# Kernel tuning notes

Measured on AMD Instinct MI355X. Metric: run time of the kernel, lower is better.

The kernel has to match this reference:

```python
import jax, jax.numpy as jnp
import numpy as np

N, B, T, E = 16384, 8, 32, 262144
D, H = 256, 8
HD = D // H

def _ln(x, g, b, eps=1e-5):
    m = x.mean(-1, keepdims=True)
    va = x.var(-1, keepdims=True)
    return (x - m) * jax.lax.rsqrt(va + eps) * g + b

def setup_inputs():
    key = jax.random.key(0)
    ks = jax.random.split(key, 40)
    rn = lambda i, sh, s=0.02: jax.random.normal(ks[i], sh, jnp.float32) * s
    inp = {}
    inp['x'] = jax.random.normal(ks[0], (N, D), jnp.float32)
    inp['edge_index'] = jax.random.randint(ks[1], (2, E), 0, N)
    inp['edge_attr'] = jax.random.normal(ks[2], (E, D), jnp.float32)
    inp['v'] = jax.random.normal(ks[3], (B, T, D), jnp.float32)
    inp['batch'] = jnp.sort(jax.random.randint(ks[4], (N,), 0, B))
    ones = lambda sh: jnp.ones(sh, jnp.float32)
    zeros = lambda sh: jnp.zeros(sh, jnp.float32)
    # LayerNorms
    inp['n1_g'], inp['n1_b'] = ones((D,)), zeros((D,))
    inp['vn_g'], inp['vn_b'] = ones((D,)), zeros((D,))
    inp['n3_g'], inp['n3_b'] = ones((D,)), zeros((D,))
    inp['n4_g'], inp['n4_b'] = ones((D,)), zeros((D,))
    # GINEConv: eps (train_eps, init 0) + MLP [D, 2D, D] with layer_norm+gelu on hidden
    inp['gine_eps'] = jnp.float32(0.0)
    inp['g_w1'], inp['g_b1'] = rn(5, (2 * D, D)), zeros((2 * D,))
    inp['g_lng'], inp['g_lnb'] = ones((2 * D,)), zeros((2 * D,))
    inp['g_w2'], inp['g_b2'] = rn(6, (D, 2 * D)), zeros((D,))
    # GatedResidual gammas (init 1e-5)
    inp['gamma1'] = jnp.full((D,), 1e-5, jnp.float32)
    inp['gamma2'] = jnp.full((D,), 1e-5, jnp.float32)
    inp['gamma3'] = jnp.full((D,), 1e-5, jnp.float32)
    # MultiheadAttention (packed in_proj)
    inp['mha_in_w'], inp['mha_in_b'] = rn(7, (3 * D, D)), zeros((3 * D,))
    inp['mha_out_w'], inp['mha_out_b'] = rn(8, (D, D)), zeros((D,))
    # node->token cross attention projections
    inp['q_w'], inp['q_b'] = rn(9, (D, D)), zeros((D,))
    inp['kv_w'], inp['kv_b'] = rn(10, (2 * D, D)), zeros((2 * D,))
    inp['o_w'], inp['o_b'] = rn(11, (D, D)), zeros((D,))
    # FFN MLP [D, 4D, D] (eval-mode batch_norm == identity with default stats)
    inp['f_w1'], inp['f_b1'] = rn(12, (4 * D, D)), zeros((4 * D,))
    inp['f_w2'], inp['f_b2'] = rn(13, (D, 4 * D)), zeros((D,))
    return inp

def reference(x, edge_index, edge_attr, v, batch,
              n1_g, n1_b, vn_g, vn_b, n3_g, n3_b, n4_g, n4_b,
              gine_eps, g_w1, g_b1, g_lng, g_lnb, g_w2, g_b2,
              gamma1, gamma2, gamma3,
              mha_in_w, mha_in_b, mha_out_w, mha_out_b,
              q_w, q_b, kv_w, kv_b, o_w, o_b,
              f_w1, f_b1, f_w2, f_b2):
    scale = HD ** -0.5
    gelu = lambda t: jax.nn.gelu(t, approximate=False)
    # --- GINEConv on norm1(x) ---
    xn = _ln(x, n1_g, n1_b)
    src, dst = edge_index[0], edge_index[1]
    msg = jax.nn.relu(xn[src] + edge_attr)                      # [E, D]
    agg = jax.ops.segment_sum(msg, dst, num_segments=N)         # [N, D]
    hin = (1.0 + gine_eps) * xn + agg
    h = gelu(_ln(hin @ g_w1.T + g_b1, g_lng, g_lnb)) @ g_w2.T + g_b2
    x = x + gamma1 * h                                          # res1 (drop_path off in eval)
    # --- token self-attention with node summary context ---
    v_res = v
    vn = _ln(v, vn_g, vn_b)
    cnt = jnp.maximum(jax.ops.segment_sum(jnp.ones((N,), x.dtype), batch, num_segments=B), 1.0)
    node_summary = jax.ops.segment_sum(x, batch, num_segments=B) / cnt[:, None]  # [B, D]
    ctx = jnp.concatenate([vn, node_summary[:, None, :]], axis=1)                # [B, T+1, D]
    wq, wk, wv = jnp.split(mha_in_w, 3, axis=0)
    bq, bk, bv = jnp.split(mha_in_b, 3, axis=0)
    qh = (vn @ wq.T + bq).reshape(B, T, H, HD)
    kh = (ctx @ wk.T + bk).reshape(B, T + 1, H, HD)
    vh = (ctx @ wv.T + bv).reshape(B, T + 1, H, HD)
    a = jax.nn.softmax(jnp.einsum('bqhd,bkhd->bhqk', qh, kh) * scale, axis=-1)
    v_upd = jnp.einsum('bhqk,bkhd->bqhd', a, vh).reshape(B, T, D) @ mha_out_w.T + mha_out_b
    v = v_res + gamma2 * v_upd                                  # res2
    # --- node -> token cross attention (gather-expand KV by batch) ---
    xn3 = _ln(x, n3_g, n3_b)
    q = (xn3 @ q_w.T + q_b).reshape(N, H, HD)
    kv = (v @ kv_w.T + kv_b).reshape(B, T, 2, H, HD)
    k, val = kv[:, :, 0], kv[:, :, 1]                           # [B, T, H, HD]
    k_exp, val_exp = k[batch], val[batch]                       # [N, T, H, HD]
    scores = jnp.einsum('nhd,nthd->nht', q, k_exp) * scale
    attn = jax.nn.softmax(scores, axis=-1)                      # scatter_softmax w/ all-zero idx == softmax over t
    attn_out = jnp.einsum('nht,nthd->nhd', attn, val_exp).reshape(N, D)
    x = x + gamma3 * (attn_out @ o_w.T + o_b)                   # res3
    # --- FFN ---
    xn4 = _ln(x, n4_g, n4_b)
    x = x + (gelu(xn4 @ f_w1.T + f_b1) @ f_w2.T + f_b2)
    return (x, v)
```

## Files before the change

### kernel.cpp

```cpp
#include <hip/hip_runtime.h>
#include <math.h>

#define NN 16384
#define EE 262144
#define BB 8
#define TT 32
#define DD 256
#define HH 8
#define HDD 32

typedef __bf16 bf16;
typedef __bf16 bf16x8 __attribute__((ext_vector_type(8)));
typedef __bf16 bf16x4 __attribute__((ext_vector_type(4)));
typedef float f32x4 __attribute__((ext_vector_type(4)));

#define GM_F32 0
#define GM_BF16 1
#define GM_GELU 2
#define GM_RES 3
#define GM_RES2 4

__device__ __forceinline__ float gelu_f(float v) {
  return 0.5f * v * (1.f + erff(v * 0.70710678118654752440f));
}

__device__ __forceinline__ void ln256(const float* __restrict__ xr,
                                      const float* __restrict__ g,
                                      const float* __restrict__ bb,
                                      bf16* __restrict__ o, float* red) {
  int t = threadIdx.x;
  float v = xr[t];
  float s = v, s2 = v * v;
#pragma unroll
  for (int off = 32; off > 0; off >>= 1) {
    s += __shfl_down(s, off, 64);
    s2 += __shfl_down(s2, off, 64);
  }
  int wv = t >> 6;
  if ((t & 63) == 0) { red[wv] = s; red[4 + wv] = s2; }
  __syncthreads();
  s = red[0] + red[1] + red[2] + red[3];
  s2 = red[4] + red[5] + red[6] + red[7];
  float m = s * (1.f / 256.f);
  float rs = rsqrtf(s2 * (1.f / 256.f) - m * m + 1e-5f);
  o[t] = (bf16)((v - m) * rs * g[t] + bb[t]);
}

struct Pro {
  const float* wsrc[9];
  bf16* wdst[9];
  int wblk[10];
  const float* x; const float* n1_g; const float* n1_b; bf16* xn;
  const float* v; const float* vn_g; const float* vn_b; bf16* vn;
  const int* batch; float* cntf;
  const int* ei; int* deg;
};

__global__ __launch_bounds__(256) void prologue(Pro p) {
  __shared__ float red[8];
  __shared__ int hist[BB];
  int b = blockIdx.x, t = threadIdx.x;
  if (b < 1280) {
    int s = 0;
    while (b >= p.wblk[s + 1]) ++s;
    int i = (b - p.wblk[s]) * 1024 + t * 4;
    const float4 f = *(const float4*)(p.wsrc[s] + i);
    bf16x4 o;
    o[0] = (bf16)f.x; o[1] = (bf16)f.y; o[2] = (bf16)f.z; o[3] = (bf16)f.w;
    *(bf16x4*)(p.wdst[s] + i) = o;
  } else if (b < 17664) {
    size_t r = b - 1280;
    ln256(p.x + r * 256, p.n1_g, p.n1_b, p.xn + r * 256, red);
  } else if (b < 17920) {
    size_t r = b - 17664;
    ln256(p.v + r * 256, p.vn_g, p.vn_b, p.vn + r * 256, red);
  } else if (b < 17984) {
    if (t < BB) hist[t] = 0;
    __syncthreads();
    int n = (b - 17920) * 256 + t;
    atomicAdd(&hist[p.batch[n]], 1);
    __syncthreads();
    if (t < BB) {
      int h = hist[t];
      if (h) atomicAdd(&p.cntf[t], (float)h);
    }
  } else {
    int e = (b - 17984) * 256 + t;
    atomicAdd(&p.deg[p.ei[EE + e]], 1);
  }
}

__global__ __launch_bounds__(1024) void scan16k(const int* __restrict__ deg,
                                                int* __restrict__ offs, int* __restrict__ woff) {
  __shared__ int part[1024];
  int t = threadIdx.x;
  int base = t * 16;
  int v[16];
  int s = 0;
#pragma unroll
  for (int j = 0; j < 16; ++j) { v[j] = deg[base + j]; s += v[j]; }
  part[t] = s;
  __syncthreads();
  for (int o = 1; o < 1024; o <<= 1) {
    int x = (t >= o) ? part[t - o] : 0;
    __syncthreads();
    part[t] += x;
    __syncthreads();
  }
  int excl = part[t] - s;
#pragma unroll
  for (int j = 0; j < 16; ++j) {
    offs[base + j] = excl;
    woff[base + j] = excl;
    excl += v[j];
  }
  if (t == 1023) offs[NN] = part[1023];
}

struct GemmP {
  const bf16* A; const bf16* W; const float* bias;
  int M, K, NC, mode;
  const float* res; const float* gamma;
  float* outf; bf16* outb;
};

__device__ __forceinline__ void gemm_core(const GemmP p, int bx, int by) {
  int wave = threadIdx.x >> 6;
  int lane = threadIdx.x & 63;
  int qd = lane >> 4;
  int l16 = lane & 15;
  int r0 = by * 128 + wave * 32;
  int c0 = bx * 64;
  int ar0 = r0 + l16;       if (ar0 >= p.M) ar0 = p.M - 1;
  int ar1 = r0 + 16 + l16;  if (ar1 >= p.M) ar1 = p.M - 1;
  const bf16* Ap0 = p.A + (size_t)ar0 * p.K + qd * 8;
  const bf16* Ap1 = p.A + (size_t)ar1 * p.K + qd * 8;
  const bf16* Wp = p.W + (size_t)(c0 + l16) * p.K + qd * 8;
  size_t K16 = (size_t)16 * p.K;
  f32x4 acc00 = {0.f, 0.f, 0.f, 0.f};
  f32x4 acc01 = acc00, acc02 = acc00, acc03 = acc00;
  f32x4 acc10 = acc00, acc11 = acc00, acc12 = acc00, acc13 = acc00;
  bf16x8 a0, a1, b0, b1, b2, b3, na0, na1, nb0, nb1, nb2, nb3;

#define GLOADS(A0, A1, B0, B1, B2, B3, kk)                \
  A0 = *(const bf16x8*)(Ap0 + (kk));                      \
  A1 = *(const bf16x8*)(Ap1 + (kk));                      \
  B0 = *(const bf16x8*)(Wp + (kk));                       \
  B1 = *(const bf16x8*)(Wp + K16 + (kk));                 \
  B2 = *(const bf16x8*)(Wp + 2 * K16 + (kk));             \
  B3 = *(const bf16x8*)(Wp + 3 * K16 + (kk));
#define GMFMAS(A0, A1, B0, B1, B2, B3)                                  \
  acc00 = __builtin_amdgcn_mfma_f32_16x16x32_bf16(A0, B0, acc00, 0, 0, 0); \
  acc01 = __builtin_amdgcn_mfma_f32_16x16x32_bf16(A0, B1, acc01, 0, 0, 0); \
  acc02 = __builtin_amdgcn_mfma_f32_16x16x32_bf16(A0, B2, acc02, 0, 0, 0); \
  acc03 = __builtin_amdgcn_mfma_f32_16x16x32_bf16(A0, B3, acc03, 0, 0, 0); \
  acc10 = __builtin_amdgcn_mfma_f32_16x16x32_bf16(A1, B0, acc10, 0, 0, 0); \
  acc11 = __builtin_amdgcn_mfma_f32_16x16x32_bf16(A1, B1, acc11, 0, 0, 0); \
  acc12 = __builtin_amdgcn_mfma_f32_16x16x32_bf16(A1, B2, acc12, 0, 0, 0); \
  acc13 = __builtin_amdgcn_mfma_f32_16x16x32_bf16(A1, B3, acc13, 0, 0, 0);

  GLOADS(a0, a1, b0, b1, b2, b3, 0)
  int k = 32;
  for (; k + 32 < p.K; k += 64) {
    GLOADS(na0, na1, nb0, nb1, nb2, nb3, k)
    GMFMAS(a0, a1, b0, b1, b2, b3)
    GLOADS(a0, a1, b0, b1, b2, b3, k + 32)
    GMFMAS(na0, na1, nb0, nb1, nb2, nb3)
  }
  GLOADS(na0, na1, nb0, nb1, nb2, nb3, k)
  GMFMAS(a0, a1, b0, b1, b2, b3)
  GMFMAS(na0, na1, nb0, nb1, nb2, nb3)
#undef GLOADS
#undef GMFMAS

  f32x4 accs[2][4] = {{acc00, acc01, acc02, acc03}, {acc10, acc11, acc12, acc13}};
#pragma unroll
  for (int s = 0; s < 2; ++s) {
#pragma unroll
    for (int c = 0; c < 4; ++c) {
      int col = c0 + c * 16 + l16;
      float bv = p.bias[col];
#pragma unroll
      for (int i = 0; i < 4; ++i) {
        int row = r0 + s * 16 + qd * 4 + i;
        if (row >= p.M) continue;
        size_t idx = (size_t)row * p.NC + col;
        float v = accs[s][c][i] + bv;
        if (p.mode == GM_F32) p.outf[idx] = v;
        else if (p.mode == GM_BF16) p.outb[idx] = (bf16)v;
        else if (p.mode == GM_GELU) p.outb[idx] = (bf16)gelu_f(v);
        else {
          float g = p.gamma ? p.gamma[col] : 1.f;
          float r = p.res[idx] + g * v;
          p.outf[idx] = r;
          if (p.mode == GM_RES2) p.outb[idx] = (bf16)r;
        }
      }
    }
  }
}

__global__ __launch_bounds__(256) void gemm_one(GemmP p, int nbx) {
  gemm_core(p, blockIdx.x % nbx, blockIdx.x / nbx);
}

__global__ __launch_bounds__(256) void csr_fill_qh(const int* __restrict__ ei,
                                                   int* __restrict__ woff,
                                                   int2* __restrict__ csr2, GemmP qp) {
  int b = blockIdx.x;
  if (b < 1024) {
    int e = b * 256 + threadIdx.x;
    int d = ei[EE + e];
    int s = ei[e];
    int p = atomicAdd(&woff[d], 1);
    csr2[p] = make_int2(e, s);
  } else {
    int l = b - 1024;
    gemm_core(qp, l % 4, l / 4);
  }
}

__global__ __launch_bounds__(256) void gine_agg(const float* __restrict__ eattr,
                                                const bf16* __restrict__ xn,
                                                const int* __restrict__ offs,
                                                const int2* __restrict__ csr2,
                                                const float* __restrict__ epsp,
                                                bf16* __restrict__ hin) {
  __shared__ f32x4 red[4][64];
  int n = blockIdx.x;
  int wave = threadIdx.x >> 6, lane = threadIdx.x & 63;
  int s0 = offs[n], s1 = offs[n + 1];
  f32x4 acc = {0.f, 0.f, 0.f, 0.f};
  int i = s0 + wave;
  int2 es = (i < s1) ? csr2[i] : make_int2(0, 0);
  for (; i < s1; i += 4) {
    int2 cur = es;
    int inext = i + 4;
    if (inext < s1) es = csr2[inext];
    float4 ea = *(const float4*)(eattr + (size_t)cur.x * DD + lane * 4);
    bf16x4 xv = *(const bf16x4*)(xn + (size_t)cur.y * DD + lane * 4);
    acc[0] += fmaxf((float)xv[0] + ea.x, 0.f);
    acc[1] += fmaxf((float)xv[1] + ea.y, 0.f);
    acc[2] += fmaxf((float)xv[2] + ea.z, 0.f);
    acc[3] += fmaxf((float)xv[3] + ea.w, 0.f);
  }
  red[wave][lane] = acc;
  __syncthreads();
  if (wave == 0) {
    f32x4 a = red[0][lane];
    f32x4 a1 = red[1][lane], a2 = red[2][lane], a3 = red[3][lane];
    bf16x4 xs = *(const bf16x4*)(xn + (size_t)n * DD + lane * 4);
    float e1 = 1.f + epsp[0];
    bf16x4 o;
#pragma unroll
    for (int j = 0; j < 4; ++j)
      o[j] = (bf16)(e1 * (float)xs[j] + a[j] + a1[j] + a2[j] + a3[j]);
    *(bf16x4*)(hin + (size_t)n * DD + lane * 4) = o;
  }
}

__global__ __launch_bounds__(256) void gemm_g1_ln(const bf16* __restrict__ A,
                                                  const bf16* __restrict__ W,
                                                  const float* __restrict__ bias,
                                                  const float* __restrict__ lng,
                                                  const float* __restrict__ lnb,
                                                  bf16* __restrict__ out) {
  __shared__ float ssum[4][32], ssum2[4][32], smm[32], smr[32];
  int w = threadIdx.x >> 6, lane = threadIdx.x & 63;
  int qd = lane >> 4, l16 = lane & 15;
  int r0 = blockIdx.x * 32;
  int c0 = w * 128;
  const bf16* Ap0 = A + (size_t)(r0 + l16) * 256 + qd * 8;
  const bf16* Ap1 = Ap0 + (size_t)16 * 256;
  const bf16* Wp = W + (size_t)(c0 + l16) * 256 + qd * 8;
  f32x4 z = {0.f, 0.f, 0.f, 0.f};
  f32x4 acc0[8], acc1[8];
#pragma unroll
  for (int cf = 0; cf < 8; ++cf) { acc0[cf] = z; acc1[cf] = z; }
  for (int k = 0; k < 256; k += 32) {
    bf16x8 a0 = *(const bf16x8*)(Ap0 + k);
    bf16x8 a1 = *(const bf16x8*)(Ap1 + k);
#pragma unroll
    for (int cf = 0; cf < 8; ++cf) {
      bf16x8 bv = *(const bf16x8*)(Wp + (size_t)cf * 16 * 256 + k);
      acc0[cf] = __builtin_amdgcn_mfma_f32_16x16x32_bf16(a0, bv, acc0[cf], 0, 0, 0);
      acc1[cf] = __builtin_amdgcn_mfma_f32_16x16x32_bf16(a1, bv, acc1[cf], 0, 0, 0);
    }
  }
#pragma unroll
  for (int cf = 0; cf < 8; ++cf) {
    float bv = bias[c0 + cf * 16 + l16];
#pragma unroll
    for (int i = 0; i < 4; ++i) { acc0[cf][i] += bv; acc1[cf][i] += bv; }
  }
#pragma unroll
  for (int s = 0; s < 2; ++s) {
#pragma unroll
    for (int i = 0; i < 4; ++i) {
      float ps = 0.f, ps2 = 0.f;
#pragma unroll
      for (int cf = 0; cf < 8; ++cf) {
        float v = s ? acc1[cf][i] : acc0[cf][i];
        ps += v; ps2 += v * v;
      }
#pragma unroll
      for (int off = 8; off > 0; off >>= 1) {
        ps += __shfl_down(ps, off, 16);
        ps2 += __shfl_down(ps2, off, 16);
      }
      if (l16 == 0) { int rib = s * 16 + qd * 4 + i; ssum[w][rib] = ps; ssum2[w][rib] = ps2; }
    }
  }
  __syncthreads();
  if (threadIdx.x < 32) {
    int rib = threadIdx.x;
    float S = ssum[0][rib] + ssum[1][rib] + ssum[2][rib] + ssum[3][rib];
    float S2 = ssum2[0][rib] + ssum2[1][rib] + ssum2[2][rib] + ssum2[3][rib];
    float m = S * (1.f / 512.f);
    smm[rib] = m;
    smr[rib] = rsqrtf(S2 * (1.f / 512.f) - m * m + 1e-5f);
  }
  __syncthreads();
#pragma unroll
  for (int s = 0; s < 2; ++s) {
#pragma unroll
    for (int cf = 0; cf < 8; ++cf) {
      int col = c0 + cf * 16 + l16;
      float g = lng[col], b = lnb[col];
#pragma unroll
      for (int i = 0; i < 4; ++i) {
        int rib = s * 16 + qd * 4 + i;
        float v = ((s ? acc1[cf][i] : acc0[cf][i]) - smm[rib]) * smr[rib] * g + b;
        out[(size_t)(r0 + rib) * 512 + col] = (bf16)gelu_f(v);
      }
    }
  }
}

struct ResLnP {
  const bf16* A; const bf16* W; const float* bias;
  const float* res; const float* gamma;
  float* resout; const float* lng; const float* lnb; bf16* lnout;
  int K; int seg; const int* batch; float* summary;
};

__global__ __launch_bounds__(256) void gemm_res_ln(ResLnP p) {
  __shared__ float ssum[4][32], ssum2[4][32], smm[32], smr[32];
  int w = threadIdx.x >> 6, lane = threadIdx.x & 63;
  int qd = lane >> 4, l16 = lane & 15;
  int r0 = blockIdx.x * 32;
  int c0 = w * 64;
  const bf16* Ap0 = p.A + (size_t)(r0 + l16) * p.K + qd * 8;
  const bf16* Ap1 = Ap0 + (size_t)16 * p.K;
  const bf16* Wp = p.W + (size_t)(c0 + l16) * p.K + qd * 8;
  size_t K16 = (size_t)16 * p.K;
  f32x4 z = {0.f, 0.f, 0.f, 0.f};
  f32x4 acc0[4], acc1[4];
#pragma unroll
  for (int cf = 0; cf < 4; ++cf) { acc0[cf] = z; acc1[cf] = z; }
  for (int k = 0; k < p.K; k += 32) {
    bf16x8 a0 = *(const bf16x8*)(Ap0 + k);
    bf16x8 a1 = *(const bf16x8*)(Ap1 + k);
#pragma unroll
    for (int cf = 0; cf < 4; ++cf) {
      bf16x8 bv = *(const bf16x8*)(Wp + cf * K16 + k);
      acc0[cf] = __builtin_amdgcn_mfma_f32_16x16x32_bf16(a0, bv, acc0[cf], 0, 0, 0);
      acc1[cf] = __builtin_amdgcn_mfma_f32_16x16x32_bf16(a1, bv, acc1[cf], 0, 0, 0);
    }
  }
  float rr0[4][4], rr1[4][4];
#pragma unroll
  for (int cf = 0; cf < 4; ++cf) {
    int col = c0 + cf * 16 + l16;
    float bv = p.bias[col], gm = p.gamma[col];
#pragma unroll
    for (int i = 0; i < 4; ++i) {
      {
        int row = r0 + qd * 4 + i;
        size_t idx = (size_t)row * 256 + col;
        float r = p.res[idx] + gm * (acc0[cf][i] + bv);
        p.resout[idx] = r; rr0[cf][i] = r;
      }
      {
        int row = r0 + 16 + qd * 4 + i;
        size_t idx = (size_t)row * 256 + col;
        float r = p.res[idx] + gm * (acc1[cf][i] + bv);
        p.resout[idx] = r; rr1[cf][i] = r;
      }
    }
  }
#pragma unroll
  for (int s = 0; s < 2; ++s) {
#pragma unroll
    for (int i = 0; i < 4; ++i) {
      float ps = 0.f, ps2 = 0.f;
#pragma unroll
      for (int cf = 0; cf < 4; ++cf) {
        float v = s ? rr1[cf][i] : rr0[cf][i];
        ps += v; ps2 += v * v;
      }
#pragma unroll
      for (int off = 8; off > 0; off >>= 1) {
        ps += __shfl_down(ps, off, 16);
        ps2 += __shfl_down(ps2, off, 16);
      }
      if (l16 == 0) { int rib = s * 16 + qd * 4 + i; ssum[w][rib] = ps; ssum2[w][rib] = ps2; }
    }
  }
  __syncthreads();
  if (threadIdx.x < 32) {
    int rib = threadIdx.x;
    float S = ssum[0][rib] + ssum[1][rib] + ssum[2][rib] + ssum[3][rib];
    float S2 = ssum2[0][rib] + ssum2[1][rib] + ssum2[2][rib] + ssum2[3][rib];
    float m = S * (1.f / 256.f);
    smm[rib] = m;
    smr[rib] = rsqrtf(S2 * (1.f / 256.f) - m * m + 1e-5f);
  }
  __syncthreads();
#pragma unroll
  for (int cf = 0; cf < 4; ++cf) {
    int col = c0 + cf * 16 + l16;
    float lg = p.lng[col], lb = p.lnb[col];
#pragma unroll
    for (int i = 0; i < 4; ++i) {
      {
        int rib = qd * 4 + i;
        p.lnout[(size_t)(r0 + rib) * 256 + col] =
            (bf16)((rr0[cf][i] - smm[rib]) * smr[rib] * lg + lb);
      }
      {
        int rib = 16 + qd * 4 + i;
        p.lnout[(size_t)(r0 + rib) * 256 + col] =
            (bf16)((rr1[cf][i] - smm[rib]) * smr[rib] * lg + lb);
      }
    }
  }
  if (p.seg) {
    int b0 = p.batch[r0], b31 = p.batch[r0 + 31];
    if (b0 == b31) {
#pragma unroll
      for (int cf = 0; cf < 4; ++cf) {
        float sl = 0.f;
#pragma unroll
        for (int i = 0; i < 4; ++i) sl += rr0[cf][i] + rr1[cf][i];
        sl += __shfl_xor(sl, 16, 64);
        sl += __shfl_xor(sl, 32, 64);
        if (qd == 0) atomicAdd(&p.summary[(size_t)b0 * 256 + c0 + cf * 16 + l16], sl);
      }
    } else {
#pragma unroll
      for (int cf = 0; cf < 4; ++cf) {
        int col = c0 + cf * 16 + l16;
#pragma unroll
        for (int i = 0; i < 4; ++i) {
          atomicAdd(&p.summary[(size_t)p.batch[r0 + qd * 4 + i] * 256 + col], rr0[cf][i]);
          atomicAdd(&p.summary[(size_t)p.batch[r0 + 16 + qd * 4 + i] * 256 + col], rr1[cf][i]);
        }
      }
    }
  }
}

__global__ __launch_bounds__(256) void mid2(const float* __restrict__ summary,
                                            const float* __restrict__ cntf,
                                            const bf16* __restrict__ vn,
                                            bf16* __restrict__ ctx,
                                            GemmP qp) {
  int b = blockIdx.x, t = threadIdx.x;
  if (b < BB * (TT + 1)) {
    int bb = b / (TT + 1), k = b % (TT + 1);
    float val;
    if (k < TT) val = (float)vn[((size_t)(bb * TT + k)) * DD + t];
    else val = summary[(size_t)bb * DD + t] / fmaxf(cntf[bb], 1.f);
    ctx[(size_t)b * DD + t] = (bf16)val;
  } else {
    int l = b - BB * (TT + 1);
    gemm_core(qp, l % 4, l / 4);
  }
}

__global__ __launch_bounds__(256) void mha_small(const float* __restrict__ qh,
                                                 const float* __restrict__ kvh,
                                                 bf16* __restrict__ vatt) {
  int b = blockIdx.x;
  int h = threadIdx.x >> 5, qi = threadIdx.x & 31;
  const float scale = 0.17677669529663687f;
  float sc[TT + 1];
  float mx = -1e30f;
  const float* qp = qh + ((size_t)(b * TT + qi)) * DD + h * HDD;
#pragma unroll
  for (int k = 0; k < TT + 1; ++k) {
    const float* kp = kvh + ((size_t)(b * (TT + 1) + k)) * 512 + h * HDD;
    float s = 0.f;
#pragma unroll
    for (int d = 0; d < HDD; ++d) s += qp[d] * kp[d];
    s *= scale;
    sc[k] = s;
    mx = fmaxf(mx, s);
  }
  float sum = 0.f;
#pragma unroll
  for (int k = 0; k < TT + 1; ++k) {
    sc[k] = __expf(sc[k] - mx);
    sum += sc[k];
  }
  float inv = 1.f / sum;
#pragma unroll
  for (int d = 0; d < HDD; ++d) {
    float o = 0.f;
#pragma unroll
    for (int k = 0; k < TT + 1; ++k)
      o += sc[k] * kvh[((size_t)(b * (TT + 1) + k)) * 512 + 256 + h * HDD + d];
    vatt[((size_t)(b * TT + qi)) * DD + h * HDD + d] = (bf16)(o * inv);
  }
}

__global__ __launch_bounds__(256) void cross_attn(const bf16* __restrict__ qx,
                                                  const float* __restrict__ kvx,
                                                  const int* __restrict__ batch,
                                                  bf16* __restrict__ attnout) {
  __shared__ float v_lds[TT * DD];
  int tid = threadIdx.x;
  int n0 = blockIdx.x * 16;
  int b0 = batch[n0];
  for (int i = tid; i < TT * DD; i += 256) {
    int t = i >> 8, c = i & 255;
    v_lds[i] = kvx[((size_t)(b0 * TT + t)) * 512 + 256 + c];
  }
  int h = tid >> 5, lt = tid & 31;
  float kreg[HDD];
  {
    const float* kp = kvx + ((size_t)(b0 * TT + lt)) * 512 + h * HDD;
#pragma unroll
    for (int d = 0; d < HDD; ++d) kreg[d] = kp[d];
  }
  __syncthreads();
  const float scale = 0.17677669529663687f;
  for (int ni = 0; ni < 16; ++ni) {
    int n = n0 + ni;
    int b = batch[n];
    const bf16* qp = qx + (size_t)n * DD + h * HDD;
    float s = 0.f;
    if (b == b0) {
#pragma unroll
      for (int d = 0; d < HDD; ++d) s += (float)qp[d] * kreg[d];
    } else {
      const float* kp = kvx + ((size_t)(b * TT + lt)) * 512 + h * HDD;
#pragma unroll
      for (int d = 0; d < HDD; ++d) s += (float)qp[d] * kp[d];
    }
    s *= scale;
    float mx = s;
#pragma unroll
    for (int o = 16; o > 0; o >>= 1) mx = fmaxf(mx, __shfl_xor(mx, o, 32));
    float e = __expf(s - mx);
    float sum = e;
#pragma unroll
    for (int o = 16; o > 0; o >>= 1) sum += __shfl_xor(sum, o, 32);
    float a = e / sum;
    float o_acc = 0.f;
    int base_lane = (h & 1) << 5;
    if (b == b0) {
#pragma unroll
      for (int t = 0; t < TT; ++t) {
        float at = __shfl(a, base_lane + t, 64);
        o_acc += at * v_lds[t * DD + h * HDD + lt];
      }
    } else {
#pragma unroll
      for (int t = 0; t < TT; ++t) {
        float at = __shfl(a, base_lane + t, 64);
        o_acc += at * kvx[((size_t)(b * TT + t)) * 512 + 256 + h * HDD + lt];
      }
    }
    attnout[(size_t)n * DD + h * HDD + lt] = (bf16)o_acc;
  }
}

extern "C" void kernel_launch(void* const* d_in, const int* in_sizes, int n_in,
                              void* d_out, int out_size, void* d_ws, size_t ws_size,
                              hipStream_t stream) {
  const float* x = (const float*)d_in[0];
  const int* ei = (const int*)d_in[1];
  const float* eattr = (const float*)d_in[2];
  const float* v = (const float*)d_in[3];
  const int* batch = (const int*)d_in[4];
  const float* n1_g = (const float*)d_in[5];
  const float* n1_b = (const float*)d_in[6];
  const float* vn_g = (const float*)d_in[7];
  const float* vn_b = (const float*)d_in[8];
  const float* n3_g = (const float*)d_in[9];
  const float* n3_b = (const float*)d_in[10];
  const float* n4_g = (const float*)d_in[11];
  const float* n4_b = (const float*)d_in[12];
  const float* gine_eps = (const float*)d_in[13];
  const float* g_w1 = (const float*)d_in[14];
  const float* g_b1 = (const float*)d_in[15];
  const float* g_lng = (const float*)d_in[16];
  const float* g_lnb = (const float*)d_in[17];
  const float* g_w2 = (const float*)d_in[18];
  const float* g_b2 = (const float*)d_in[19];
  const float* gamma1 = (const float*)d_in[20];
  const float* gamma2 = (const float*)d_in[21];
  const float* gamma3 = (const float*)d_in[22];
  const float* mha_in_w = (const float*)d_in[23];
  const float* mha_in_b = (const float*)d_in[24];
  const float* mha_out_w = (const float*)d_in[25];
  const float* mha_out_b = (const float*)d_in[26];
  const float* q_w = (const float*)d_in[27];
  const float* q_b = (const float*)d_in[28];
  const float* kv_w = (const float*)d_in[29];
  const float* kv_b = (const float*)d_in[30];
  const float* o_w = (const float*)d_in[31];
  const float* o_b = (const float*)d_in[32];
  const float* f_w1 = (const float*)d_in[33];
  const float* f_b1 = (const float*)d_in[34];
  const float* f_w2 = (const float*)d_in[35];
  const float* f_b2 = (const float*)d_in[36];

  float* out_x = (float*)d_out;
  float* out_v = (float*)d_out + (size_t)NN * DD;

  char* wsp = (char*)d_ws;
  size_t off = 0;
  auto alloc = [&](size_t bytes) -> void* {
    void* p = wsp + off;
    off += (bytes + 255) & ~(size_t)255;
    return p;
  };
  float* t1f = (float*)alloc(33554432);
  bf16* u_bf = (bf16*)t1f;
  bf16* xn_bf = (bf16*)alloc(8388608);
  bf16* qx_bf = xn_bf;
  bf16* t1g_bf = (bf16*)alloc(16777216);
  float* x2f = (float*)t1g_bf;
  float* x1f = (float*)alloc(16777216);
  bf16* hin_bf = (bf16*)alloc(8388608);
  bf16* xn3_bf = hin_bf;
  bf16* att_bf = (bf16*)alloc(8388608);
  bf16* xn4_bf = att_bf;
  int* deg = (int*)alloc(NN * 4);
  float* summary = (float*)alloc(BB * DD * 4);
  float* cntf = (float*)alloc(BB * 4);
  int* offs = (int*)alloc((NN + 1) * 4);
  int* woff = (int*)alloc(NN * 4);
  int2* csr2 = (int2*)alloc((size_t)EE * 8);
  bf16* vn_bf = (bf16*)alloc(BB * TT * DD * 2);
  bf16* ctx_bf = (bf16*)alloc(BB * (TT + 1) * DD * 2);
  float* qhf = (float*)alloc(BB * TT * DD * 4);
  float* kvhf = (float*)alloc(BB * (TT + 1) * 512 * 4);
  bf16* vatt_bf = (bf16*)alloc(BB * TT * DD * 2);
  bf16* vout_bf = (bf16*)alloc(BB * TT * DD * 2);
  float* kvxf = (float*)alloc(BB * TT * 512 * 4);
  bf16* wbuf = (bf16*)alloc((size_t)1310720 * 2);

  bf16* g_w1b = wbuf;
  bf16* g_w2b = g_w1b + 131072;
  bf16* mha_in_wb = g_w2b + 131072;
  bf16* q_wb = mha_in_wb + 196608;
  bf16* kv_wb = q_wb + 65536;
  bf16* o_wb = kv_wb + 131072;
  bf16* f_w1b = o_wb + 65536;
  bf16* f_w2b = f_w1b + 262144;
  bf16* mha_out_wb = f_w2b + 262144;

  hipMemsetAsync(deg, 0, NN * 4 + BB * DD * 4 + 256, stream);

  Pro pr;
  pr.wsrc[0] = g_w1; pr.wdst[0] = g_w1b;
  pr.wsrc[1] = g_w2; pr.wdst[1] = g_w2b;
  pr.wsrc[2] = mha_in_w; pr.wdst[2] = mha_in_wb;
  pr.wsrc[3] = mha_out_w; pr.wdst[3] = mha_out_wb;
  pr.wsrc[4] = q_w; pr.wdst[4] = q_wb;
  pr.wsrc[5] = kv_w; pr.wdst[5] = kv_wb;
  pr.wsrc[6] = o_w; pr.wdst[6] = o_wb;
  pr.wsrc[7] = f_w1; pr.wdst[7] = f_w1b;
  pr.wsrc[8] = f_w2; pr.wdst[8] = f_w2b;
  int bs[10] = {0, 128, 256, 448, 512, 576, 704, 768, 1024, 1280};
  for (int i = 0; i < 10; ++i) pr.wblk[i] = bs[i];
  pr.x = x; pr.n1_g = n1_g; pr.n1_b = n1_b; pr.xn = xn_bf;
  pr.v = v; pr.vn_g = vn_g; pr.vn_b = vn_b; pr.vn = vn_bf;
  pr.batch = batch; pr.cntf = cntf;
  pr.ei = ei; pr.deg = deg;
  prologue<<<19008, 256, 0, stream>>>(pr);

  scan16k<<<1, 1024, 0, stream>>>(deg, offs, woff);

  GemmP j_qh = {vn_bf, mha_in_wb, mha_in_b, BB * TT, 256, 256, GM_F32,
                nullptr, nullptr, qhf, nullptr};
  csr_fill_qh<<<1024 + 8, 256, 0, stream>>>(ei, woff, csr2, j_qh);

  gine_agg<<<NN, 256, 0, stream>>>(eattr, xn_bf, offs, csr2, gine_eps, hin_bf);

  gemm_g1_ln<<<NN / 32, 256, 0, stream>>>(hin_bf, g_w1b, g_b1, g_lng, g_lnb, t1g_bf);

  ResLnP j_g2 = {t1g_bf, g_w2b, g_b2, x, gamma1, x1f, n3_g, n3_b, xn3_bf,
                 512, 1, batch, summary};
  gemm_res_ln<<<NN / 32, 256, 0, stream>>>(j_g2);

  GemmP j_q = {xn3_bf, q_wb, q_b, NN, 256, 256, GM_BF16, nullptr, nullptr, nullptr, qx_bf};
  mid2<<<BB * (TT + 1) + 512, 256, 0, stream>>>(summary, cntf, vn_bf, ctx_bf, j_q);

  GemmP j_kvh = {ctx_bf, mha_in_wb + (size_t)256 * 256, mha_in_b + 256, BB * (TT + 1), 256, 512,
                 GM_F32, nullptr, nullptr, kvhf, nullptr};
  gemm_one<<<24, 256, 0, stream>>>(j_kvh, 8);

  mha_small<<<BB, 256, 0, stream>>>(qhf, kvhf, vatt_bf);

  GemmP j_mo = {vatt_bf, mha_out_wb, mha_out_b, BB * TT, 256, 256, GM_RES2, v, gamma2, out_v, vout_bf};
  gemm_one<<<8, 256, 0, stream>>>(j_mo, 4);

  GemmP j_kv = {vout_bf, kv_wb, kv_b, BB * TT, 256, 512, GM_F32, nullptr, nullptr, kvxf, nullptr};
  gemm_one<<<16, 256, 0, stream>>>(j_kv, 8);

  cross_attn<<<NN / 16, 256, 0, stream>>>(qx_bf, kvxf, batch, att_bf);

  ResLnP j_o = {att_bf, o_wb, o_b, x1f, gamma3, x2f, n4_g, n4_b, xn4_bf,
                256, 0, nullptr, nullptr};
  gemm_res_ln<<<NN / 32, 256, 0, stream>>>(j_o);

  GemmP j_f1 = {xn4_bf, f_w1b, f_b1, NN, 256, 1024, GM_GELU, nullptr, nullptr, nullptr, u_bf};
  gemm_one<<<2048, 256, 0, stream>>>(j_f1, 16);

  GemmP j_f2 = {u_bf, f_w2b, f_b2, NN, 1024, 256, GM_RES, x2f, nullptr, out_x, nullptr};
  gemm_one<<<512, 256, 0, stream>>>(j_f2, 4);
}
```

Baseline: 914.1 us.

## Fuse FFN GEMMs via LDS, use wave-per-row LN and aggregation

Merges the two FFN GEMMs into one kernel that keeps the GELU hidden tile (32x1024 bf16) in shared memory, so the hidden activation never goes through global memory. The prologue LayerNorm now gives each wave one row with float4 loads and shuffle-only reductions, dropping the block-level sync. gine_agg gives each wave one node, removing the LDS cross-wave reduction. The trade-offs are about 66KB of LDS per block and 32 accumulator vectors per thread, which lowers occupancy. Per-node aggregation also becomes serial within a wave, so high-degree nodes have less parallelism.

```diff
diff --git a/kernel.cpp b/kernel.cpp
--- a/kernel.cpp
+++ b/kernel.cpp
@@ -24,26 +24,29 @@
   return 0.5f * v * (1.f + erff(v * 0.70710678118654752440f));
 }
 
-__device__ __forceinline__ void ln256(const float* __restrict__ xr,
-                                      const float* __restrict__ g,
-                                      const float* __restrict__ bb,
-                                      bf16* __restrict__ o, float* red) {
-  int t = threadIdx.x;
-  float v = xr[t];
-  float s = v, s2 = v * v;
+__device__ __forceinline__ void ln256w(const float* __restrict__ xr,
+                                       const float* __restrict__ g,
+                                       const float* __restrict__ bb,
+                                       bf16* __restrict__ o) {
+  int lane = threadIdx.x & 63;
+  float4 v = *(const float4*)(xr + lane * 4);
+  float s = v.x + v.y + v.z + v.w;
+  float s2 = v.x * v.x + v.y * v.y + v.z * v.z + v.w * v.w;
 #pragma unroll
   for (int off = 32; off > 0; off >>= 1) {
-    s += __shfl_down(s, off, 64);
-    s2 += __shfl_down(s2, off, 64);
-  }
-  int wv = t >> 6;
-  if ((t & 63) == 0) { red[wv] = s; red[4 + wv] = s2; }
-  __syncthreads();
-  s = red[0] + red[1] + red[2] + red[3];
-  s2 = red[4] + red[5] + red[6] + red[7];
+    s += __shfl_xor(s, off, 64);
+    s2 += __shfl_xor(s2, off, 64);
+  }
   float m = s * (1.f / 256.f);
   float rs = rsqrtf(s2 * (1.f / 256.f) - m * m + 1e-5f);
-  o[t] = (bf16)((v - m) * rs * g[t] + bb[t]);
+  float4 gg = *(const float4*)(g + lane * 4);
+  float4 bv = *(const float4*)(bb + lane * 4);
+  bf16x4 ov;
+  ov[0] = (bf16)((v.x - m) * rs * gg.x + bv.x);
+  ov[1] = (bf16)((v.y - m) * rs * gg.y + bv.y);
+  ov[2] = (bf16)((v.z - m) * rs * gg.z + bv.z);
+  ov[3] = (bf16)((v.w - m) * rs * gg.w + bv.w);
+  *(bf16x4*)(o + lane * 4) = ov;
 }
 
 struct Pro {
@@ -57,9 +60,9 @@
 };
 
 __global__ __launch_bounds__(256) void prologue(Pro p) {
-  __shared__ float red[8];
   __shared__ int hist[BB];
   int b = blockIdx.x, t = threadIdx.x;
+  int wave = t >> 6;
   if (b < 1280) {
     int s = 0;
     while (b >= p.wblk[s + 1]) ++s;
@@ -68,16 +71,16 @@
     bf16x4 o;
     o[0] = (bf16)f.x; o[1] = (bf16)f.y; o[2] = (bf16)f.z; o[3] = (bf16)f.w;
     *(bf16x4*)(p.wdst[s] + i) = o;
-  } else if (b < 17664) {
-    size_t r = b - 1280;
-    ln256(p.x + r * 256, p.n1_g, p.n1_b, p.xn + r * 256, red);
-  } else if (b < 17920) {
-    size_t r = b - 17664;
-    ln256(p.v + r * 256, p.vn_g, p.vn_b, p.vn + r * 256, red);
-  } else if (b < 17984) {
+  } else if (b < 5376) {
+    size_t r = (size_t)(b - 1280) * 4 + wave;
+    ln256w(p.x + r * 256, p.n1_g, p.n1_b, p.xn + r * 256);
+  } else if (b < 5440) {
+    size_t r = (size_t)(b - 5376) * 4 + wave;
+    ln256w(p.v + r * 256, p.vn_g, p.vn_b, p.vn + r * 256);
+  } else if (b < 5504) {
     if (t < BB) hist[t] = 0;
     __syncthreads();
-    int n = (b - 17920) * 256 + t;
+    int n = (b - 5440) * 256 + t;
     atomicAdd(&hist[p.batch[n]], 1);
     __syncthreads();
     if (t < BB) {
@@ -85,7 +88,7 @@
       if (h) atomicAdd(&p.cntf[t], (float)h);
     }
   } else {
-    int e = (b - 17984) * 256 + t;
+    int e = (b - 5504) * 256 + t;
     atomicAdd(&p.deg[p.ei[EE + e]], 1);
   }
 }
@@ -226,17 +229,15 @@
                                                 const int2* __restrict__ csr2,
                                                 const float* __restrict__ epsp,
                                                 bf16* __restrict__ hin) {
-  __shared__ f32x4 red[4][64];
-  int n = blockIdx.x;
   int wave = threadIdx.x >> 6, lane = threadIdx.x & 63;
+  int n = blockIdx.x * 4 + wave;
   int s0 = offs[n], s1 = offs[n + 1];
   f32x4 acc = {0.f, 0.f, 0.f, 0.f};
-  int i = s0 + wave;
+  int i = s0;
   int2 es = (i < s1) ? csr2[i] : make_int2(0, 0);
-  for (; i < s1; i += 4) {
+  for (; i < s1; ++i) {
     int2 cur = es;
-    int inext = i + 4;
-    if (inext < s1) es = csr2[inext];
+    if (i + 1 < s1) es = csr2[i + 1];
     float4 ea = *(const float4*)(eattr + (size_t)cur.x * DD + lane * 4);
     bf16x4 xv = *(const bf16x4*)(xn + (size_t)cur.y * DD + lane * 4);
     acc[0] += fmaxf((float)xv[0] + ea.x, 0.f);
@@ -244,19 +245,13 @@
     acc[2] += fmaxf((float)xv[2] + ea.z, 0.f);
     acc[3] += fmaxf((float)xv[3] + ea.w, 0.f);
   }
-  red[wave][lane] = acc;
-  __syncthreads();
-  if (wave == 0) {
-    f32x4 a = red[0][lane];
-    f32x4 a1 = red[1][lane], a2 = red[2][lane], a3 = red[3][lane];
-    bf16x4 xs = *(const bf16x4*)(xn + (size_t)n * DD + lane * 4);
-    float e1 = 1.f + epsp[0];
-    bf16x4 o;
-#pragma unroll
-    for (int j = 0; j < 4; ++j)
-      o[j] = (bf16)(e1 * (float)xs[j] + a[j] + a1[j] + a2[j] + a3[j]);
-    *(bf16x4*)(hin + (size_t)n * DD + lane * 4) = o;
-  }
+  bf16x4 xs = *(const bf16x4*)(xn + (size_t)n * DD + lane * 4);
+  float e1 = 1.f + epsp[0];
+  bf16x4 o;
+#pragma unroll
+  for (int j = 0; j < 4; ++j)
+    o[j] = (bf16)(e1 * (float)xs[j] + acc[j]);
+  *(bf16x4*)(hin + (size_t)n * DD + lane * 4) = o;
 }
 
 __global__ __launch_bounds__(256) void gemm_g1_ln(const bf16* __restrict__ A,
@@ -456,6 +451,83 @@
           atomicAdd(&p.summary[(size_t)p.batch[r0 + qd * 4 + i] * 256 + col], rr0[cf][i]);
           atomicAdd(&p.summary[(size_t)p.batch[r0 + 16 + qd * 4 + i] * 256 + col], rr1[cf][i]);
         }
+      }
+    }
+  }
+}
+
+__global__ __launch_bounds__(256) void gemm_ffn(const bf16* __restrict__ A,
+                                                const bf16* __restrict__ W1,
+                                                const float* __restrict__ b1,
+                                                const bf16* __restrict__ W2,
+                                                const float* __restrict__ b2,
+                                                const float* __restrict__ res,
+                                                float* __restrict__ outx) {
+  __shared__ bf16 t_lds[32 * 1032];
+  int w = threadIdx.x >> 6, lane = threadIdx.x & 63;
+  int qd = lane >> 4, l16 = lane & 15;
+  int r0 = blockIdx.x * 32;
+  {
+    int c0 = w * 256;
+    const bf16* Ap0 = A + (size_t)(r0 + l16) * 256 + qd * 8;
+    const bf16* Ap1 = Ap0 + (size_t)16 * 256;
+    const bf16* Wp = W1 + (size_t)(c0 + l16) * 256 + qd * 8;
+    f32x4 z = {0.f, 0.f, 0.f, 0.f};
+    f32x4 acc0[16], acc1[16];
+#pragma unroll
+    for (int cf = 0; cf < 16; ++cf) { acc0[cf] = z; acc1[cf] = z; }
+    for (int k = 0; k < 256; k += 32) {
+      bf16x8 a0 = *(const bf16x8*)(Ap0 + k);
+      bf16x8 a1 = *(const bf16x8*)(Ap1 + k);
+#pragma unroll
+      for (int cf = 0; cf < 16; ++cf) {
+        bf16x8 bv = *(const bf16x8*)(Wp + (size_t)cf * 16 * 256 + k);
+        acc0[cf] = __builtin_amdgcn_mfma_f32_16x16x32_bf16(a0, bv, acc0[cf], 0, 0, 0);
+        acc1[cf] = __builtin_amdgcn_mfma_f32_16x16x32_bf16(a1, bv, acc1[cf], 0, 0, 0);
+      }
+    }
+#pragma unroll
+    for (int cf = 0; cf < 16; ++cf) {
+      int col = c0 + cf * 16 + l16;
+      float bv = b1[col];
+#pragma unroll
+      for (int i = 0; i < 4; ++i) {
+        int rib0 = qd * 4 + i, rib1 = 16 + qd * 4 + i;
+        t_lds[rib0 * 1032 + col] = (bf16)gelu_f(acc0[cf][i] + bv);
+        t_lds[rib1 * 1032 + col] = (bf16)gelu_f(acc1[cf][i] + bv);
+      }
+    }
+  }
+  __syncthreads();
+  {
+    int c2 = w * 64;
+    const bf16* Wp2 = W2 + (size_t)(c2 + l16) * 1024 + qd * 8;
+    const bf16* lp0 = t_lds + l16 * 1032 + qd * 8;
+    const bf16* lp1 = t_lds + (16 + l16) * 1032 + qd * 8;
+    f32x4 z = {0.f, 0.f, 0.f, 0.f};
+    f32x4 acc0[4], acc1[4];
+#pragma unroll
+    for (int cf = 0; cf < 4; ++cf) { acc0[cf] = z; acc1[cf] = z; }
+    for (int k = 0; k < 1024; k += 32) {
+      bf16x8 a0 = *(const bf16x8*)(lp0 + k);
+      bf16x8 a1 = *(const bf16x8*)(lp1 + k);
+#pragma unroll
+      for (int cf = 0; cf < 4; ++cf) {
+        bf16x8 bv = *(const bf16x8*)(Wp2 + (size_t)cf * 16 * 1024 + k);
+        acc0[cf] = __builtin_amdgcn_mfma_f32_16x16x32_bf16(a0, bv, acc0[cf], 0, 0, 0);
+        acc1[cf] = __builtin_amdgcn_mfma_f32_16x16x32_bf16(a1, bv, acc1[cf], 0, 0, 0);
+      }
+    }
+#pragma unroll
+    for (int cf = 0; cf < 4; ++cf) {
+      int col = c2 + cf * 16 + l16;
+      float bv = b2[col];
+#pragma unroll
+      for (int i = 0; i < 4; ++i) {
+        int row0 = r0 + qd * 4 + i, row1 = row0 + 16;
+        size_t i0 = (size_t)row0 * 256 + col, i1 = (size_t)row1 * 256 + col;
+        outx[i0] = res[i0] + acc0[cf][i] + bv;
+        outx[i1] = res[i1] + acc1[cf][i] + bv;
       }
     }
   }
@@ -629,7 +701,6 @@
     return p;
   };
   float* t1f = (float*)alloc(33554432);
-  bf16* u_bf = (bf16*)t1f;
   bf16* xn_bf = (bf16*)alloc(8388608);
   bf16* qx_bf = xn_bf;
   bf16* t1g_bf = (bf16*)alloc(16777216);
@@ -653,6 +724,7 @@
   bf16* vout_bf = (bf16*)alloc(BB * TT * DD * 2);
   float* kvxf = (float*)alloc(BB * TT * 512 * 4);
   bf16* wbuf = (bf16*)alloc((size_t)1310720 * 2);
+  (void)t1f;
 
   bf16* g_w1b = wbuf;
   bf16* g_w2b = g_w1b + 131072;
@@ -682,7 +754,7 @@
   pr.v = v; pr.vn_g = vn_g; pr.vn_b = vn_b; pr.vn = vn_bf;
   pr.batch = batch; pr.cntf = cntf;
   pr.ei = ei; pr.deg = deg;
-  prologue<<<19008, 256, 0, stream>>>(pr);
+  prologue<<<6528, 256, 0, stream>>>(pr);
 
   scan16k<<<1, 1024, 0, stream>>>(deg, offs, woff);
 
@@ -690,7 +762,7 @@
                 nullptr, nullptr, qhf, nullptr};
   csr_fill_qh<<<1024 + 8, 256, 0, stream>>>(ei, woff, csr2, j_qh);
 
-  gine_agg<<<NN, 256, 0, stream>>>(eattr, xn_bf, offs, csr2, gine_eps, hin_bf);
+  gine_agg<<<NN / 4, 256, 0, stream>>>(eattr, xn_bf, offs, csr2, gine_eps, hin_bf);
 
   gemm_g1_ln<<<NN / 32, 256, 0, stream>>>(hin_bf, g_w1b, g_b1, g_lng, g_lnb, t1g_bf);
 
@@ -719,9 +791,5 @@
                 256, 0, nullptr, nullptr};
   gemm_res_ln<<<NN / 32, 256, 0, stream>>>(j_o);
 
-  GemmP j_f1 = {xn4_bf, f_w1b, f_b1, NN, 256, 1024, GM_GELU, nullptr, nullptr, nullptr, u_bf};
-  gemm_one<<<2048, 256, 0, stream>>>(j_f1, 16);
-
-  GemmP j_f2 = {u_bf, f_w2b, f_b2, NN, 1024, 256, GM_RES, x2f, nullptr, out_x, nullptr};
-  gemm_one<<<512, 256, 0, stream>>>(j_f2, 4);
-}
+  gemm_ffn<<<NN / 32, 256, 0, stream>>>(xn4_bf, f_w1b, f_b1, f_w2b, f_b2, x2f, out_x);
+}
```

Measured after the change: 888.7 us. 2.8% less time.
